# Performance work log

Hardware: AMD Instinct MI355X
Metric: run time of the kernel (lower is better)

## Reference

```python
import jax, jax.numpy as jnp
import numpy as np
from jax import lax

B, NMEAS, M, LAYER_NUM = 2048, 128, 256, 10
CLAMP_MIN, CLAMP_MAX = 1e-6, 100.0
EPS_S = 1e-6


def _conv2d(x, w, b):
    y = lax.conv_general_dilated(x, w, (1, 1), 'SAME', dimension_numbers=('NCHW', 'OIHW', 'NCHW'))
    return y + b[None, :, None, None]


def _conv1d(x, w, b):
    y = lax.conv_general_dilated(x, w, (1,), 'SAME', dimension_numbers=('NCH', 'OIH', 'NCH'))
    return y + b[None, :, None]


def setup_inputs():
    key = jax.random.key(0)
    ks = jax.random.split(key, 12)
    s = 1.0 / np.sqrt(2.0 * NMEAS)  # ~unit-norm dictionary columns
    return {
        'Yr': jax.random.normal(ks[0], (B, 1, NMEAS, 1), jnp.float32),
        'Yi': jax.random.normal(ks[1], (B, 1, NMEAS, 1), jnp.float32),
        'Ar': s * jax.random.normal(ks[2], (NMEAS, M), jnp.float32),
        'Ai': s * jax.random.normal(ks[3], (NMEAS, M), jnp.float32),
        'conv1_w': 0.1 * jax.random.normal(ks[4], (32, 2, 3, 3), jnp.float32),
        'conv1_b': jnp.zeros((32,), jnp.float32),
        'conv2_w': 0.1 * jax.random.normal(ks[5], (64, 32, 3, 3), jnp.float32),
        'conv2_b': jnp.zeros((64,), jnp.float32),
        'hc_w': 0.1 * jax.random.normal(ks[6], (LAYER_NUM - 1, 64, 3), jnp.float32),
        'hc_b': jnp.zeros((LAYER_NUM - 1,), jnp.float32),
        'hd_w': 0.1 * jax.random.normal(ks[7], (LAYER_NUM - 1, 64, 3), jnp.float32),
        'hd_b': jnp.zeros((LAYER_NUM - 1,), jnp.float32),
        'hT_w': 0.1 * jax.random.normal(ks[8], (LAYER_NUM, 64, 3), jnp.float32),
        'hT_b': jnp.zeros((LAYER_NUM,), jnp.float32),
        'a0': jnp.asarray(1.0, jnp.float32),
        'b0': jnp.asarray(1.0, jnp.float32),
    }


def _hypernet(ay, c1w, c1b, c2w, c2b, hcw, hcb, hdw, hdb, hTw, hTb):
    # ay: [B, 2, M]; batch acts as image width (context)
    x_img = jnp.transpose(ay, (1, 2, 0))[None]              # [1, 2, M, B]
    f = jax.nn.relu(_conv2d(x_img, c1w, c1b))               # [1, 32, M, B]
    f = jax.nn.relu(_conv2d(f, c2w, c2b))                   # [1, 64, M, B]
    f = jnp.mean(f, axis=2)                                 # AdaptiveAvgPool2d((1,None)) -> [1, 64, B]
    c = jnp.abs(_conv1d(f, hcw, hcb))[0].T                  # [B, L-1]
    d = jnp.abs(_conv1d(f, hdw, hdb))[0].T                  # [B, L-1]
    T = jnp.abs(_conv1d(f, hTw, hTb))[0].T                  # [B, L]
    c = jnp.clip(c, CLAMP_MIN, CLAMP_MAX)
    d = jnp.maximum(d, CLAMP_MIN)
    T = jnp.clip(T, CLAMP_MIN, CLAMP_MAX)
    return c, d, T


def _forward(Yr, Yi, Ar, Ai, conv1_w, conv1_b, conv2_w, conv2_b,
             hc_w, hc_b, hd_w, hd_b, hT_w, hT_b, a0, b0):
    Y = (Yr + 1j * Yi).astype(jnp.complex64)                # [B,1,Nmeas,1]
    A = (Ar + 1j * Ai).astype(jnp.complex64)                # [Nmeas,M]
    AT = A.conj().T                                         # [M,Nmeas]
    AA = AT @ A                                             # [M,M] Hermitian
    AY = jnp.matmul(AT, Y)                                  # [B,1,M,1]
    b = Y.shape[0]
    n = Y.shape[2]
    ay = jnp.concatenate([AY.real.reshape(b, 1, -1), AY.imag.reshape(b, 1, -1)], axis=1)  # [B,2,M]
    c, d, T = _hypernet(ay, conv1_w, conv1_b, conv2_w, conv2_b,
                        hc_w, hc_b, hd_w, hd_b, hT_w, hT_b)
    D = jnp.real(jnp.diagonal(AA))[None, None, :, None]     # diag of Hermitian AA is real; [1,1,M,1]
    eps = (a0 / b0).astype(jnp.complex64) * jnp.ones((b, 1, 1, 1), jnp.complex64)
    Lam = ((c[:, 0] / d[:, 0])[:, None, None, None] * jnp.ones((1, 1, M, 1), jnp.float32)).astype(jnp.complex64)
    U = jnp.zeros((b, 1, M, 1), jnp.complex64)
    a = a0 + n
    for k in range(LAYER_NUM - 1):
        Tk = T[:, k][:, None, None, None]
        # fused SBL/VAMP mean update
        U = eps * (Tk * U - jnp.matmul(AA, U) + AY) / (eps * Tk + Lam + EPS_S)
        Sigma = 1.0 / (eps * D + Lam + EPS_S)
        r = Y - jnp.matmul(A, U)
        eps1 = jnp.sum(r.real ** 2 + r.imag ** 2, axis=(2, 3), keepdims=True)  # ||.||_F^2
        eps2 = jnp.sum(D * Sigma, axis=(2, 3), keepdims=True)
        eps = a / (b0 + eps1 + eps2 + EPS_S)
        Lam = (c[:, k][:, None, None, None] + 1.0) / (
            d[:, k][:, None, None, None] + jnp.abs(U) ** 2 + Sigma + EPS_S)
    Tk = T[:, LAYER_NUM - 1][:, None, None, None]
    U = eps * (Tk * U - jnp.matmul(AA, U) + AY) / (eps * Tk + Lam + EPS_S)
    Ua = jnp.abs(U)
    Ua = Ua / (jnp.max(Ua) + 1e-8)
    return Ua, c, d, T


def reference(Yr, Yi, Ar, Ai, conv1_w, conv1_b, conv2_w, conv2_b,
              hc_w, hc_b, hd_w, hd_b, hT_w, hT_b, a0, b0):
    Ua, c, d, T = _forward(Yr, Yi, Ar, Ai, conv1_w, conv1_b, conv2_w, conv2_b,
                           hc_w, hc_b, hd_w, hd_b, hT_w, hT_b, a0, b0)
    # original returns the last batch row of c/d/T (detached diagnostics)
    return Ua, c[-1:, :], d[-1:, :], T[-1:, :]
```

## Files before the change

### kernel.cpp

```cpp
#include <hip/hip_runtime.h>
#include <math.h>

#define B_N   2048
#define NM    128
#define M_N   256
#define LNUM  10
#define EPS_Sf 1e-6f

typedef _Float16 half8 __attribute__((ext_vector_type(8)));
typedef float floatx4 __attribute__((ext_vector_type(4)));

__device__ __forceinline__ float frcp(float x) { return __builtin_amdgcn_rcpf(x); }

static constexpr size_t o_AA  = 0;
static constexpr size_t o_D   = o_AA  + 131072;
static constexpr size_t o_yn  = o_D   + 256;
static constexpr size_t o_AY  = o_yn  + 2048;
static constexpr size_t o_AYt = o_AY  + 1048576;
static constexpr size_t o_w2t = o_AYt + 1048576;
static constexpr size_t o_z1  = o_w2t + 18432;
static constexpr size_t o_fp  = o_z1  + 16777216;
static constexpr size_t o_f   = o_fp  + 2097152;
static constexpr size_t o_c   = o_f   + 131072;
static constexpr size_t o_dd  = o_c   + 18432;
static constexpr size_t o_T   = o_dd  + 18432;
static constexpr size_t o_Ua  = o_T   + 20480;
static constexpr size_t o_gm  = o_Ua  + 524288;

#define Z1T_RS (2050 * 32)

__global__ void k_pre(const float* __restrict__ Ar, const float* __restrict__ Ai,
                      const float* __restrict__ Yr, const float* __restrict__ Yi,
                      const float* __restrict__ w2, float* __restrict__ ws) {
    __shared__ float sb[2048];
    int blk = blockIdx.x;
    int tid = threadIdx.x;
    if (blk < 256) {
        float* cr = sb; float* ci = sb + NM;
        int i = blk, j = tid;
        if (j < NM) { cr[j] = Ar[j * M_N + i]; ci[j] = Ai[j * M_N + i]; }
        __syncthreads();
        float sr = 0.f, si = 0.f;
        for (int n = 0; n < NM; ++n) {
            float ar = Ar[n * M_N + j], ai = Ai[n * M_N + j];
            sr += cr[n] * ar + ci[n] * ai;
            si += cr[n] * ai - ci[n] * ar;
        }
        _Float16* A16 = (_Float16*)(ws + o_AA);
        size_t off = ((size_t)((i >> 4) * 8 + (j >> 5)) * 64
                      + (size_t)(((j >> 3) & 3) * 16 + (i & 15))) * 8 + (j & 7);
        A16[off]         = (_Float16)sr;
        A16[65536 + off] = (_Float16)si;
        if (j == i) ws[o_D + i] = sr;
        if (i == 0 && j == 0) *(unsigned int*)(ws + o_gm) = 0u;
    } else if (blk < 328) {
        int i = (blk - 256) * 256 + tid;
        if (i < 64 * 32 * 9) {
            int oc = i / 288, r = i % 288;
            int ic = r / 9, kk = r % 9;
            _Float16* Wa = (_Float16*)(ws + o_w2t);
            Wa[((size_t)oc * 9 + kk) * 32 + ic] = (_Float16)w2[i];
        }
    } else {
        float2* Ys = (float2*)sb;
        int bb0 = (blk - 328) * 8;
        for (int i = tid; i < 8 * NM; i += 256) {
            int g = i >> 7, n = i & 127;
            Ys[g * NM + n] = make_float2(Yr[(size_t)(bb0 + g) * NM + n],
                                         Yi[(size_t)(bb0 + g) * NM + n]);
        }
        __syncthreads();
        if (tid < 8) {
            float s = 0.f;
            for (int n = 0; n < NM; ++n) { float2 y = Ys[tid * NM + n]; s += y.x * y.x + y.y * y.y; }
            ws[o_yn + bb0 + tid] = s;
        }
        int m = tid;
        float accr[8], acci[8];
#pragma unroll
        for (int g = 0; g < 8; ++g) { accr[g] = 0.f; acci[g] = 0.f; }
        for (int n = 0; n < NM; ++n) {
            float ar = Ar[n * M_N + m], ai = Ai[n * M_N + m];
#pragma unroll
            for (int g = 0; g < 8; ++g) {
                float2 y = Ys[g * NM + n];
                accr[g] += ar * y.x + ai * y.y;
                acci[g] += ar * y.y - ai * y.x;
            }
        }
#pragma unroll
        for (int g = 0; g < 8; ++g) {
            ws[o_AYt + (size_t)m * B_N + (bb0 + g)] = accr[g];
            ws[o_AYt + 524288 + (size_t)m * B_N + (bb0 + g)] = acci[g];
        }
    }
}

__global__ void k_conv1(const float* __restrict__ w1, const float* __restrict__ b1,
                        float* __restrict__ ws) {
    __shared__ float w1s[576], b1s[32];
    int tid = threadIdx.x;
    for (int i = tid; i < 576; i += 256) w1s[i] = w1[i];
    if (tid < 32) b1s[tid] = b1[tid];
    __syncthreads();
    int gidx = blockIdx.x * 256 + tid;
    int b = gidx & (B_N - 1), m = gidx >> 11;
    const float* xr = ws + o_AYt;
    float x[2][3][3];
#pragma unroll
    for (int c = 0; c < 2; ++c)
#pragma unroll
        for (int dm = 0; dm < 3; ++dm) {
            int mm = m + dm - 1;
#pragma unroll
            for (int db = 0; db < 3; ++db) {
                int bb = b + db - 1;
                x[c][dm][db] = (mm >= 0 && mm < M_N && bb >= 0 && bb < B_N)
                                 ? xr[(size_t)c * 524288 + (size_t)mm * B_N + bb] : 0.f;
            }
        }
    _Float16* z1t = (_Float16*)(ws + o_z1);
    _Float16 zv[32];
    for (int oc = 0; oc < 32; ++oc) {
        float acc = b1s[oc];
#pragma unroll
        for (int c = 0; c < 2; ++c)
#pragma unroll
            for (int dm = 0; dm < 3; ++dm)
#pragma unroll
                for (int db = 0; db < 3; ++db)
                    acc += x[c][dm][db] * w1s[oc * 18 + c * 9 + dm * 3 + db];
        zv[oc] = (_Float16)fmaxf(acc, 0.f);
    }
    _Float16* dst = z1t + (size_t)(m + 1) * Z1T_RS + (size_t)(b + 1) * 32;
#pragma unroll
    for (int v = 0; v < 4; ++v) *(half8*)(dst + v * 8) = *(half8*)(zv + v * 8);
    half8 z8 = (half8)((_Float16)0.f);
    if (m == 0) {
        _Float16* d2 = z1t + (size_t)(b + 1) * 32;
#pragma unroll
        for (int v = 0; v < 4; ++v) *(half8*)(d2 + v * 8) = z8;
        if (b == 0) { _Float16* d3 = z1t;
#pragma unroll
            for (int v = 0; v < 4; ++v) *(half8*)(d3 + v * 8) = z8; }
        if (b == B_N - 1) { _Float16* d3 = z1t + (size_t)2049 * 32;
#pragma unroll
            for (int v = 0; v < 4; ++v) *(half8*)(d3 + v * 8) = z8; }
    }
    if (m == M_N - 1) {
        _Float16* d2 = z1t + (size_t)257 * Z1T_RS + (size_t)(b + 1) * 32;
#pragma unroll
        for (int v = 0; v < 4; ++v) *(half8*)(d2 + v * 8) = z8;
        if (b == 0) { _Float16* d3 = z1t + (size_t)257 * Z1T_RS;
#pragma unroll
            for (int v = 0; v < 4; ++v) *(half8*)(d3 + v * 8) = z8; }
        if (b == B_N - 1) { _Float16* d3 = z1t + (size_t)257 * Z1T_RS + (size_t)2049 * 32;
#pragma unroll
            for (int v = 0; v < 4; ++v) *(half8*)(d3 + v * 8) = z8; }
    }
    if (b == 0) {
        _Float16* d2 = z1t + (size_t)(m + 1) * Z1T_RS;
#pragma unroll
        for (int v = 0; v < 4; ++v) *(half8*)(d2 + v * 8) = z8;
    }
    if (b == B_N - 1) {
        _Float16* d2 = z1t + (size_t)(m + 1) * Z1T_RS + (size_t)2049 * 32;
#pragma unroll
        for (int v = 0; v < 4; ++v) *(half8*)(d2 + v * 8) = z8;
    }
}

#define MFMA16(A,Bv,C) C = __builtin_amdgcn_mfma_f32_16x16x32_f16(A, Bv, C, 0, 0, 0)
__global__ void __launch_bounds__(128)
k_conv2m(const float* __restrict__ b2, float* __restrict__ ws) {
    int tid = threadIdx.x;
    int lane = tid & 63, wv = tid >> 6;
    int col = lane & 15, quad = lane >> 4;
    int bt = blockIdx.x & 127, g = blockIdx.x >> 7;
    int b0 = bt * 16, m0 = g * 16;
    int oc0w = wv * 32;
    const _Float16* z1t = (const _Float16*)(ws + o_z1);
    const _Float16* Wa  = (const _Float16*)(ws + o_w2t);

    half8 Af[2][9];
#pragma unroll
    for (int t = 0; t < 2; ++t)
#pragma unroll
        for (int kk = 0; kk < 9; ++kk)
            Af[t][kk] = *(const half8*)(Wa + ((size_t)(oc0w + t * 16 + col) * 9 + kk) * 32 + quad * 8);
    float bias[2][4];
#pragma unroll
    for (int t = 0; t < 2; ++t)
#pragma unroll
        for (int r = 0; r < 4; ++r)
            bias[t][r] = b2[oc0w + t * 16 + quad * 4 + r];

    const _Float16* zb = z1t + (size_t)(b0 + col) * 32 + quad * 8;
    half8 Bf[3][3];
#pragma unroll
    for (int ph = 0; ph < 3; ++ph)
#pragma unroll
        for (int db = 0; db < 3; ++db)
            Bf[ph][db] = *(const half8*)(zb + (size_t)(m0 + ph) * Z1T_RS + (size_t)db * 32);

    floatx4 facc[2];
    facc[0] = (floatx4){0.f, 0.f, 0.f, 0.f};
    facc[1] = (floatx4){0.f, 0.f, 0.f, 0.f};

#pragma unroll
    for (int mm = 0; mm < 16; ++mm) {
        floatx4 a0 = (floatx4){0.f, 0.f, 0.f, 0.f};
        floatx4 a1 = (floatx4){0.f, 0.f, 0.f, 0.f};
#pragma unroll
        for (int dm = 0; dm < 3; ++dm) {
            int ph = (mm + dm) % 3;
#pragma unroll
            for (int db = 0; db < 3; ++db) {
                MFMA16(Af[0][dm * 3 + db], Bf[ph][db], a0);
                MFMA16(Af[1][dm * 3 + db], Bf[ph][db], a1);
            }
        }
#pragma unroll
        for (int r = 0; r < 4; ++r) {
            facc[0][r] += fmaxf(a0[r] + bias[0][r], 0.f);
            facc[1][r] += fmaxf(a1[r] + bias[1][r], 0.f);
        }
        if (mm < 15) {
            int ph = mm % 3;
#pragma unroll
            for (int db = 0; db < 3; ++db)
                Bf[ph][db] = *(const half8*)(zb + (size_t)(m0 + mm + 3) * Z1T_RS + (size_t)db * 32);
        }
    }
    float* fp = ws + o_fp + (size_t)g * 131072;
#pragma unroll
    for (int t = 0; t < 2; ++t)
#pragma unroll
        for (int r = 0; r < 4; ++r)
            fp[(size_t)(oc0w + t * 16 + quad * 4 + r) * B_N + b0 + col] = facc[t][r];
}

__global__ void k_fred(float* __restrict__ ws) {
    size_t i = (size_t)blockIdx.x * 256 + threadIdx.x;
    float s = 0.f;
    for (int p = 0; p < 16; ++p) s += ws[o_fp + (size_t)p * 131072 + i];
    ws[o_f + i] = s * (1.f / 256.f);
}

__global__ void k_cdt(const float* __restrict__ hcw, const float* __restrict__ hcb,
                      const float* __restrict__ hdw, const float* __restrict__ hdb,
                      const float* __restrict__ hTw, const float* __restrict__ hTb,
                      float* __restrict__ ws, float* __restrict__ out) {
    int l = blockIdx.x >> 3;
    int b = (blockIdx.x & 7) * 256 + threadIdx.x;
    const float* f = ws + o_f;
    const float* w; float bi; int li, kind;
    if (l < 9)       { kind = 0; li = l;      w = hcw + (size_t)li * 192; bi = hcb[li]; }
    else if (l < 18) { kind = 1; li = l - 9;  w = hdw + (size_t)li * 192; bi = hdb[li]; }
    else             { kind = 2; li = l - 18; w = hTw + (size_t)li * 192; bi = hTb[li]; }
    __shared__ float wsm[192];
    for (int i = threadIdx.x; i < 192; i += 256) wsm[i] = w[i];
    __syncthreads();
    float acc = bi;
    bool okL = (b > 0), okR = (b < B_N - 1);
    for (int ic = 0; ic < 64; ++ic) {
        const float* fr = f + (size_t)ic * B_N + b;
        float fm1 = okL ? fr[-1] : 0.f;
        float f0  = fr[0];
        float fp1 = okR ? fr[1] : 0.f;
        acc += fm1 * wsm[ic * 3] + f0 * wsm[ic * 3 + 1] + fp1 * wsm[ic * 3 + 2];
    }
    float v = fmaxf(fabsf(acc), 1e-6f);
    if (kind != 1) v = fminf(v, 100.f);
    if (kind == 0)      { ws[o_c  + (size_t)b * 9  + li] = v; if (b == B_N - 1) out[524288 + li] = v; }
    else if (kind == 1) { ws[o_dd + (size_t)b * 9  + li] = v; if (b == B_N - 1) out[524297 + li] = v; }
    else                { ws[o_T  + (size_t)b * 10 + li] = v; if (b == B_N - 1) out[524306 + li] = v; }
}

__global__ void __launch_bounds__(1024, 4)
k_iter(const float* __restrict__ a0p, const float* __restrict__ b0p, float* __restrict__ ws) {
    __shared__ __align__(16) _Float16 Ubf[2][8][64][8];
    __shared__ __align__(16) float redv[16][52];
    __shared__ __align__(16) float UaT[16][260];
    __shared__ float redm[16];
    int tid = threadIdx.x;
    int lane = tid & 63, w = tid >> 6;
    int col = lane & 15, quad = lane >> 4;
    int b = blockIdx.x * 16 + col;
    const _Float16* Af = (const _Float16*)(ws + o_AA);
    float a0 = a0p[0], b0v = b0p[0];
    float atot = a0 + (float)NM;
    float yn = ws[o_yn + b];
    float eps = a0 / b0v;
    float Tv[10], cv[9], dvv[9];
#pragma unroll
    for (int i = 0; i < 10; ++i) Tv[i] = ws[o_T + (size_t)b * 10 + i];
#pragma unroll
    for (int i = 0; i < 9; ++i) cv[i] = ws[o_c + (size_t)b * 9 + i];
#pragma unroll
    for (int i = 0; i < 9; ++i) dvv[i] = ws[o_dd + (size_t)b * 9 + i];
    float lam0 = cv[0] * frcp(dvv[0]);
    half8 Ar8[8], Ai8[8];
#pragma unroll
    for (int ks = 0; ks < 8; ++ks) {
        const _Float16* ab = Af + ((size_t)(w * 8 + ks) * 64 + lane) * 8;
        Ar8[ks] = *(const half8*)(ab);
        Ai8[ks] = *(const half8*)(ab + 65536);
    }
    float Dv[4], ayr[4], ayi[4], lam[4], Ur[4], Ui[4], sg[4], wr_[4], wi_[4];
#pragma unroll
    for (int r = 0; r < 4; ++r) {
        int m = w * 16 + quad * 4 + r;
        Dv[r] = ws[o_D + m];
        ayr[r] = ws[o_AYt + (size_t)m * B_N + b];
        ayi[r] = ws[o_AYt + 524288 + (size_t)m * B_N + b];
        lam[r] = lam0;
        Ur[r] = 0.f; Ui[r] = 0.f; wr_[r] = 0.f; wi_[r] = 0.f;
    }
    int ksw = w >> 1;
    int quadD = (w & 1) * 2 + (quad >> 1);
    int laneD = quadD * 16 + col;
    int eb = (quad & 1) * 4;
    for (int k = 0; k < LNUM; ++k) {
        float Tk = Tv[k];
#pragma unroll
        for (int r = 0; r < 4; ++r) {
            float iv = eps * frcp(fmaf(eps, Tk, lam[r] + EPS_Sf));
            Ur[r] = iv * (Tk * Ur[r] - wr_[r] + ayr[r]);
            Ui[r] = iv * (Tk * Ui[r] - wi_[r] + ayi[r]);
        }
        if (k == LNUM - 1) break;
        {
            union { _Float16 h[4]; unsigned long long u; } c0, c2;
#pragma unroll
            for (int r = 0; r < 4; ++r) {
                c0.h[r] = (_Float16)Ur[r];
                c2.h[r] = (_Float16)Ui[r];
            }
            *(unsigned long long*)&Ubf[0][ksw][laneD][eb] = c0.u;
            *(unsigned long long*)&Ubf[1][ksw][laneD][eb] = c2.u;
        }
        __syncthreads();
        floatx4 wrp = (floatx4){0.f, 0.f, 0.f, 0.f};
        floatx4 wrn = (floatx4){0.f, 0.f, 0.f, 0.f};
        floatx4 wia1 = (floatx4){0.f, 0.f, 0.f, 0.f};
        floatx4 wia2 = (floatx4){0.f, 0.f, 0.f, 0.f};
#pragma unroll
        for (int ks = 0; ks < 8; ++ks) {
            half8 urh = *(const half8*)&Ubf[0][ks][lane][0];
            half8 uih = *(const half8*)&Ubf[1][ks][lane][0];
            MFMA16(Ar8[ks], urh, wrp);
            MFMA16(Ai8[ks], uih, wrn);
            MFMA16(Ar8[ks], uih, wia1);
            MFMA16(Ai8[ks], urh, wia2);
        }
        float p1 = 0.f, p2 = 0.f, p3 = 0.f;
#pragma unroll
        for (int r = 0; r < 4; ++r) {
            wr_[r] = wrp[r] - wrn[r];
            wi_[r] = wia1[r] + wia2[r];
            sg[r] = frcp(fmaf(eps, Dv[r], lam[r] + EPS_Sf));
            p1 += ayr[r] * Ur[r] + ayi[r] * Ui[r];
            p2 += Ur[r] * wr_[r] + Ui[r] * wi_[r];
            p3 += Dv[r] * sg[r];
        }
        p1 += __shfl_xor(p1, 16); p1 += __shfl_xor(p1, 32);
        p2 += __shfl_xor(p2, 16); p2 += __shfl_xor(p2, 32);
        p3 += __shfl_xor(p3, 16); p3 += __shfl_xor(p3, 32);
        if (lane < 16) {
            redv[col][w * 3]     = p1;
            redv[col][w * 3 + 1] = p2;
            redv[col][w * 3 + 2] = p3;
        }
        __syncthreads();
        float s[3] = {0.f, 0.f, 0.f};
#pragma unroll
        for (int j = 0; j < 12; ++j) {
            floatx4 v4 = *(const floatx4*)&redv[col][j * 4];
#pragma unroll
            for (int e = 0; e < 4; ++e) s[(j * 4 + e) % 3] += v4[e];
        }
        float eps1 = fmaxf(yn - 2.f * s[0] + s[1], 0.f);
        eps = atot * frcp(b0v + eps1 + s[2] + EPS_Sf);
        float ck1 = cv[k] + 1.f;
        float dk = dvv[k];
#pragma unroll
        for (int r = 0; r < 4; ++r)
            lam[r] = ck1 * frcp(dk + Ur[r] * Ur[r] + Ui[r] * Ui[r] + sg[r] + EPS_Sf);
    }
    float4 v;
    v.x = sqrtf(Ur[0] * Ur[0] + Ui[0] * Ui[0]);
    v.y = sqrtf(Ur[1] * Ur[1] + Ui[1] * Ui[1]);
    v.z = sqrtf(Ur[2] * Ur[2] + Ui[2] * Ui[2]);
    v.w = sqrtf(Ur[3] * Ur[3] + Ui[3] * Ui[3]);
    *(float4*)&UaT[col][w * 16 + quad * 4] = v;
    __syncthreads();
    float4 v2 = *(const float4*)&UaT[w][lane * 4];
    *(float4*)&ws[o_Ua + (size_t)(blockIdx.x * 16 + w) * M_N + lane * 4] = v2;
    float lm = fmaxf(fmaxf(v2.x, v2.y), fmaxf(v2.z, v2.w));
#pragma unroll
    for (int off = 32; off >= 1; off >>= 1) lm = fmaxf(lm, __shfl_xor(lm, off));
    if (lane == 0) redm[w] = lm;
    __syncthreads();
    if (tid == 0) {
        float mx = redm[0];
#pragma unroll
        for (int i = 1; i < 16; ++i) mx = fmaxf(mx, redm[i]);
        atomicMax((unsigned int*)(ws + o_gm), __float_as_uint(mx));
    }
}

__global__ void k_norm(const float* __restrict__ ws, float* __restrict__ out) {
    size_t i = (size_t)blockIdx.x * 256 + threadIdx.x;
    float gm = __uint_as_float(*(const unsigned int*)(ws + o_gm));
    out[i] = ws[o_Ua + i] / (gm + 1e-8f);
}

extern "C" void kernel_launch(void* const* d_in, const int* in_sizes, int n_in,
                              void* d_out, int out_size, void* d_ws, size_t ws_size,
                              hipStream_t stream) {
    (void)in_sizes; (void)n_in; (void)out_size; (void)ws_size;
    const float* Yr  = (const float*)d_in[0];
    const float* Yi  = (const float*)d_in[1];
    const float* Ar  = (const float*)d_in[2];
    const float* Ai  = (const float*)d_in[3];
    const float* w1  = (const float*)d_in[4];
    const float* b1  = (const float*)d_in[5];
    const float* w2  = (const float*)d_in[6];
    const float* b2  = (const float*)d_in[7];
    const float* hcw = (const float*)d_in[8];
    const float* hcb = (const float*)d_in[9];
    const float* hdw = (const float*)d_in[10];
    const float* hdb = (const float*)d_in[11];
    const float* hTw = (const float*)d_in[12];
    const float* hTb = (const float*)d_in[13];
    const float* a0  = (const float*)d_in[14];
    const float* b0  = (const float*)d_in[15];
    float* ws = (float*)d_ws;
    float* out = (float*)d_out;

    k_pre   <<<584, 256, 0, stream>>>(Ar, Ai, Yr, Yi, w2, ws);
    k_conv1 <<<2048, 256, 0, stream>>>(w1, b1, ws);
    k_conv2m<<<2048, 128, 0, stream>>>(b2, ws);
    k_fred  <<<512, 256, 0, stream>>>(ws);
    k_cdt   <<<224, 256, 0, stream>>>(hcw, hcb, hdw, hdb, hTw, hTb, ws, out);
    k_iter  <<<128, 1024, 0, stream>>>(a0, b0, ws);
    k_norm  <<<2048, 256, 0, stream>>>(ws, out);
}
```

Baseline: 229.7 us.

## Fuse conv1 into conv2 MFMA kernel with LDS halo recompute

```diff
diff --git a/kernel.cpp b/kernel.cpp
--- a/kernel.cpp
+++ b/kernel.cpp
@@ -26,8 +26,6 @@
 static constexpr size_t o_T   = o_dd  + 18432;
 static constexpr size_t o_Ua  = o_T   + 20480;
 static constexpr size_t o_gm  = o_Ua  + 524288;
-
-#define Z1T_RS (2050 * 32)
 
 __global__ void k_pre(const float* __restrict__ Ar, const float* __restrict__ Ai,
                       const float* __restrict__ Yr, const float* __restrict__ Yi,
@@ -96,92 +94,32 @@
     }
 }
 
-__global__ void k_conv1(const float* __restrict__ w1, const float* __restrict__ b1,
-                        float* __restrict__ ws) {
-    __shared__ float w1s[576], b1s[32];
-    int tid = threadIdx.x;
-    for (int i = tid; i < 576; i += 256) w1s[i] = w1[i];
-    if (tid < 32) b1s[tid] = b1[tid];
-    __syncthreads();
-    int gidx = blockIdx.x * 256 + tid;
-    int b = gidx & (B_N - 1), m = gidx >> 11;
-    const float* xr = ws + o_AYt;
-    float x[2][3][3];
-#pragma unroll
-    for (int c = 0; c < 2; ++c)
-#pragma unroll
-        for (int dm = 0; dm < 3; ++dm) {
-            int mm = m + dm - 1;
-#pragma unroll
-            for (int db = 0; db < 3; ++db) {
-                int bb = b + db - 1;
-                x[c][dm][db] = (mm >= 0 && mm < M_N && bb >= 0 && bb < B_N)
-                                 ? xr[(size_t)c * 524288 + (size_t)mm * B_N + bb] : 0.f;
-            }
-        }
-    _Float16* z1t = (_Float16*)(ws + o_z1);
-    _Float16 zv[32];
-    for (int oc = 0; oc < 32; ++oc) {
-        float acc = b1s[oc];
-#pragma unroll
-        for (int c = 0; c < 2; ++c)
-#pragma unroll
-            for (int dm = 0; dm < 3; ++dm)
-#pragma unroll
-                for (int db = 0; db < 3; ++db)
-                    acc += x[c][dm][db] * w1s[oc * 18 + c * 9 + dm * 3 + db];
-        zv[oc] = (_Float16)fmaxf(acc, 0.f);
-    }
-    _Float16* dst = z1t + (size_t)(m + 1) * Z1T_RS + (size_t)(b + 1) * 32;
-#pragma unroll
-    for (int v = 0; v < 4; ++v) *(half8*)(dst + v * 8) = *(half8*)(zv + v * 8);
-    half8 z8 = (half8)((_Float16)0.f);
-    if (m == 0) {
-        _Float16* d2 = z1t + (size_t)(b + 1) * 32;
-#pragma unroll
-        for (int v = 0; v < 4; ++v) *(half8*)(d2 + v * 8) = z8;
-        if (b == 0) { _Float16* d3 = z1t;
-#pragma unroll
-            for (int v = 0; v < 4; ++v) *(half8*)(d3 + v * 8) = z8; }
-        if (b == B_N - 1) { _Float16* d3 = z1t + (size_t)2049 * 32;
-#pragma unroll
-            for (int v = 0; v < 4; ++v) *(half8*)(d3 + v * 8) = z8; }
-    }
-    if (m == M_N - 1) {
-        _Float16* d2 = z1t + (size_t)257 * Z1T_RS + (size_t)(b + 1) * 32;
-#pragma unroll
-        for (int v = 0; v < 4; ++v) *(half8*)(d2 + v * 8) = z8;
-        if (b == 0) { _Float16* d3 = z1t + (size_t)257 * Z1T_RS;
-#pragma unroll
-            for (int v = 0; v < 4; ++v) *(half8*)(d3 + v * 8) = z8; }
-        if (b == B_N - 1) { _Float16* d3 = z1t + (size_t)257 * Z1T_RS + (size_t)2049 * 32;
-#pragma unroll
-            for (int v = 0; v < 4; ++v) *(half8*)(d3 + v * 8) = z8; }
-    }
-    if (b == 0) {
-        _Float16* d2 = z1t + (size_t)(m + 1) * Z1T_RS;
-#pragma unroll
-        for (int v = 0; v < 4; ++v) *(half8*)(d2 + v * 8) = z8;
-    }
-    if (b == B_N - 1) {
-        _Float16* d2 = z1t + (size_t)(m + 1) * Z1T_RS + (size_t)2049 * 32;
-#pragma unroll
-        for (int v = 0; v < 4; ++v) *(half8*)(d2 + v * 8) = z8;
-    }
-}
-
 #define MFMA16(A,Bv,C) C = __builtin_amdgcn_mfma_f32_16x16x32_f16(A, Bv, C, 0, 0, 0)
 __global__ void __launch_bounds__(128)
-k_conv2m(const float* __restrict__ b2, float* __restrict__ ws) {
+k_conv12(const float* __restrict__ w1, const float* __restrict__ b1,
+         const float* __restrict__ b2, float* __restrict__ ws) {
+    __shared__ float xw[2][20][20];
+    __shared__ float w1s[576], b1s[32];
+    __shared__ __align__(16) _Float16 zt[18][18][32];
     int tid = threadIdx.x;
     int lane = tid & 63, wv = tid >> 6;
     int col = lane & 15, quad = lane >> 4;
     int bt = blockIdx.x & 127, g = blockIdx.x >> 7;
     int b0 = bt * 16, m0 = g * 16;
+
+    for (int i = tid; i < 576; i += 128) w1s[i] = w1[i];
+    if (tid < 32) b1s[tid] = b1[tid];
+    const float* xr = ws + o_AYt;
+    for (int i = tid; i < 800; i += 128) {
+        int c = i / 400, r = (i % 400) / 20, cc = i % 20;
+        int gm = m0 - 2 + r, gb = b0 - 2 + cc;
+        float v = 0.f;
+        if (gm >= 0 && gm < M_N && gb >= 0 && gb < B_N)
+            v = xr[(size_t)c * 524288 + (size_t)gm * B_N + gb];
+        xw[c][r][cc] = v;
+    }
     int oc0w = wv * 32;
-    const _Float16* z1t = (const _Float16*)(ws + o_z1);
-    const _Float16* Wa  = (const _Float16*)(ws + o_w2t);
-
+    const _Float16* Wa = (const _Float16*)(ws + o_w2t);
     half8 Af[2][9];
 #pragma unroll
     for (int t = 0; t < 2; ++t)
@@ -194,19 +132,42 @@
 #pragma unroll
         for (int r = 0; r < 4; ++r)
             bias[t][r] = b2[oc0w + t * 16 + quad * 4 + r];
-
-    const _Float16* zb = z1t + (size_t)(b0 + col) * 32 + quad * 8;
+    __syncthreads();
+
+    for (int p = tid; p < 324; p += 128) {
+        int ml = p / 18, bl = p % 18;
+        int gm = m0 - 1 + ml, gb = b0 - 1 + bl;
+        _Float16 zv[32];
+        if (gm >= 0 && gm < M_N && gb >= 0 && gb < B_N) {
+            for (int oc = 0; oc < 32; ++oc) {
+                float acc = b1s[oc];
+#pragma unroll
+                for (int c = 0; c < 2; ++c)
+#pragma unroll
+                    for (int dm = 0; dm < 3; ++dm)
+#pragma unroll
+                        for (int db = 0; db < 3; ++db)
+                            acc += xw[c][ml + dm][bl + db] * w1s[oc * 18 + c * 9 + dm * 3 + db];
+                zv[oc] = (_Float16)fmaxf(acc, 0.f);
+            }
+        } else {
+#pragma unroll
+            for (int oc = 0; oc < 32; ++oc) zv[oc] = (_Float16)0.f;
+        }
+#pragma unroll
+        for (int v = 0; v < 4; ++v) *(half8*)&zt[ml][bl][v * 8] = *(half8*)(zv + v * 8);
+    }
+    __syncthreads();
+
     half8 Bf[3][3];
 #pragma unroll
     for (int ph = 0; ph < 3; ++ph)
 #pragma unroll
         for (int db = 0; db < 3; ++db)
-            Bf[ph][db] = *(const half8*)(zb + (size_t)(m0 + ph) * Z1T_RS + (size_t)db * 32);
-
+            Bf[ph][db] = *(const half8*)&zt[ph][col + db][quad * 8];
     floatx4 facc[2];
     facc[0] = (floatx4){0.f, 0.f, 0.f, 0.f};
     facc[1] = (floatx4){0.f, 0.f, 0.f, 0.f};
-
 #pragma unroll
     for (int mm = 0; mm < 16; ++mm) {
         floatx4 a0 = (floatx4){0.f, 0.f, 0.f, 0.f};
@@ -229,7 +190,7 @@
             int ph = mm % 3;
 #pragma unroll
             for (int db = 0; db < 3; ++db)
-                Bf[ph][db] = *(const half8*)(zb + (size_t)(m0 + mm + 3) * Z1T_RS + (size_t)db * 32);
+                Bf[ph][db] = *(const half8*)&zt[mm + 3][col + db][quad * 8];
         }
     }
     float* fp = ws + o_fp + (size_t)g * 131072;
@@ -440,8 +401,7 @@
     float* out = (float*)d_out;
 
     k_pre   <<<584, 256, 0, stream>>>(Ar, Ai, Yr, Yi, w2, ws);
-    k_conv1 <<<2048, 256, 0, stream>>>(w1, b1, ws);
-    k_conv2m<<<2048, 128, 0, stream>>>(b2, ws);
+    k_conv12<<<2048, 128, 0, stream>>>(w1, b1, b2, ws);
     k_fred  <<<512, 256, 0, stream>>>(ws);
     k_cdt   <<<224, 256, 0, stream>>>(hcw, hcb, hdw, hdb, hTw, hTb, ws, out);
     k_iter  <<<128, 1024, 0, stream>>>(a0, b0, ws);
```

After: 317.8 us. 38.4% more time.
